# Performance work log

Measured on AMD Instinct MI355X. Metric: run time of the kernel, lower is better.

Reference implementation:

```python
import jax, jax.numpy as jnp
import numpy as np
from jax import lax

# ---- fixed configuration (matches init_kwargs / input_specs) ----
L, E, V, F, HU, HL, S = 32, 1024, 2048, 8, 128, 2, 7
D0, D1R, D1E = 512, 129, 640
D = S + 1                      # path dimension = num_slices + 1
SIGLEN = D + D * D + D * D * D # iisignature.siglength(8, 3) = 584
FINAL = F * 2 * SIGLEN         # 9344
EPS = 1e-5                     # BatchNorm eps


def _bn(x, g, b):
    # BatchNorm1d in training mode: biased batch statistics over axis 0
    mu = x.mean(0)
    var = x.var(0)
    return (x - mu) / jnp.sqrt(var + EPS) * g + b


def _mlp(x, Win, bin_, gin, betain, Wh, bh, gh, betah, Wout, bout, gout, betaout):
    # eigf: Linear+BN+ReLU blocks, 1 -> HU -> ... -> HU -> 1
    h = jax.nn.relu(_bn(x @ Win.T + bin_, gin, betain))
    for l in range(HL):
        h = jax.nn.relu(_bn(h @ Wh[l].T + bh[l], gh[l], betah[l]))
    o = jax.nn.relu(_bn(h @ Wout.T + bout, gout, betaout))
    return o[:, 0]


# ---- path signature, level 3, via Chen's identity (replaces iisignature.sig) ----
def _seg(dx):
    s1 = dx
    s2 = jnp.outer(s1, dx).reshape(-1) * 0.5
    s3 = jnp.outer(s2, dx).reshape(-1) / 3.0
    return (s1, s2, s3)


def _chen(Sg, T):
    s1, s2, s3 = Sg
    t1, t2, t3 = T
    r1 = s1 + t1
    r2 = s2 + t2 + jnp.outer(s1, t1).reshape(-1)
    r3 = s3 + t3 + jnp.outer(s1, t2).reshape(-1) + jnp.outer(s2, t1).reshape(-1)
    return (r1, r2, r3)


def _sig3(path):  # path [P, D] -> [SIGLEN]
    dX = path[1:] - path[:-1]

    def step(Sg, dx):
        return _chen(Sg, _seg(dx)), None

    Sg, _ = lax.scan(step, _seg(dX[0]), dX[1:])
    return jnp.concatenate(Sg)


def _diagram_sig(vals, W_proj, b_proj):
    # Conv1d(1, S, kernel=2, stride=2) == pairwise projection; then sort, prepend time axis
    pairs = vals.reshape(-1, 2)                      # [P, 2]
    P = pairs.shape[0]
    proj = jnp.einsum('pk,sk->sp', pairs, W_proj[:, 0, :]) + b_proj[:, None]  # [S, P]
    proj = jnp.sort(proj, axis=-1)
    t = jnp.arange(P, dtype=vals.dtype) / (P * (P + 1) / 2.0)
    path = jnp.concatenate([t[None, :], proj], axis=0).T  # [P, D]
    return _sig3(path)


def setup_inputs() -> dict:
    key = jax.random.key(0)
    ks = iter(jax.random.split(key, 16))
    nrm = lambda kk, shp, sc: jax.random.normal(kk, shp, jnp.float32) * sc
    inp = {
        "eigenvalues": jax.random.uniform(next(ks), (L, E), jnp.float32),
        "eigenvectors_sq": jax.random.uniform(next(ks), (L, E, V), jnp.float32) / E,
        "dgm0": jax.random.randint(next(ks), (L, F, D0), 0, V, jnp.int32),
        "dgm1rel": jax.random.randint(next(ks), (L, F, D1R), 0, V, jnp.int32),
        "dgm1ext": jax.random.randint(next(ks), (L, F, D1E), 0, V, jnp.int32),
        "mlp_Win": nrm(next(ks), (F, HU, 1), 1.0),
        "mlp_bin": jnp.zeros((F, HU), jnp.float32),
        "mlp_gin": jnp.ones((F, HU), jnp.float32),
        "mlp_betain": jnp.zeros((F, HU), jnp.float32),
        "mlp_Wh": nrm(next(ks), (F, HL, HU, HU), 1.0 / np.sqrt(HU)),
        "mlp_bh": jnp.zeros((F, HL, HU), jnp.float32),
        "mlp_gh": jnp.ones((F, HL, HU), jnp.float32),
        "mlp_betah": jnp.zeros((F, HL, HU), jnp.float32),
        "mlp_Wout": nrm(next(ks), (F, 1, HU), 1.0 / np.sqrt(HU)),
        "mlp_bout": jnp.zeros((F, 1), jnp.float32),
        "mlp_gout": jnp.ones((F, 1), jnp.float32),
        "mlp_betaout": jnp.zeros((F, 1), jnp.float32),
        "W_proj": nrm(next(ks), (S, 1, 2), 0.7),
        "b_proj": jnp.zeros((S,), jnp.float32),
        "W_fin": nrm(next(ks), (1, FINAL), 1.0 / np.sqrt(FINAL)),
        "b_fin": jnp.zeros((1,), jnp.float32),
        "g_fin": jnp.ones((1,), jnp.float32),
        "beta_fin": jnp.zeros((1,), jnp.float32),
    }
    return inp


def reference(eigenvalues, eigenvectors_sq, dgm0, dgm1rel, dgm1ext,
              mlp_Win, mlp_bin, mlp_gin, mlp_betain,
              mlp_Wh, mlp_bh, mlp_gh, mlp_betah,
              mlp_Wout, mlp_bout, mlp_gout, mlp_betaout,
              W_proj, b_proj, W_fin, b_fin, g_fin, beta_fin):
    flat = eigenvalues.reshape(-1, 1)  # [L*E, 1], sample-major like the torch flatten
    evs = jax.vmap(lambda *p: _mlp(flat, *p))(
        mlp_Win, mlp_bin, mlp_gin, mlp_betain,
        mlp_Wh, mlp_bh, mlp_gh, mlp_betah,
        mlp_Wout, mlp_bout, mlp_gout, mlp_betaout)  # [F, L*E]
    # per-sample filtration values: evs_transformed[:, slice_i] @ eigvecsq_i
    f = jnp.einsum('fle,lev->lfv', evs.reshape(F, L, E), eigenvectors_sq)  # [L, F, V]
    fv = f.reshape(L * F, V)
    d0 = jnp.take_along_axis(fv, dgm0.reshape(L * F, D0), axis=1)
    rel = jnp.take_along_axis(fv, dgm1rel.reshape(L * F, D1R), axis=1)
    # torch.arange(len-1, 0, -1): reversed, dropping element 0
    Dgm0 = jnp.concatenate([d0, rel[:, 1:][:, ::-1]], axis=1)  # [L*F, 640]
    Dgm1 = jnp.take_along_axis(fv, dgm1ext.reshape(L * F, D1E), axis=1)
    sig0 = jax.vmap(lambda v: _diagram_sig(v, W_proj, b_proj))(Dgm0)  # [L*F, SIGLEN]
    sig1 = jax.vmap(lambda v: _diagram_sig(v, W_proj, b_proj))(Dgm1)
    x = jnp.concatenate([sig0, sig1], axis=-1).reshape(L, FINAL)
    out = x @ W_fin.T + b_fin  # dropout p=0.0 -> identity
    return _bn(out, g_fin, beta_fin)  # [L, 1]
```

## Files before the change

### kernel.cpp

```cpp
#include <hip/hip_runtime.h>
#include <cfloat>
#include <math.h>

#define N_SAMP 32768
#define FF 8
#define HU 128
#define EE 1024
#define VV 2048
#define PP 320
#define SIGLEN 584
#define FINAL_W 9344

typedef unsigned short u16;
typedef unsigned int u32;
typedef short s16x8 __attribute__((ext_vector_type(8)));
typedef float f32x4 __attribute__((ext_vector_type(4)));

__device__ __forceinline__ u16 f2bf(float v) {
  u32 u = __float_as_uint(v);
  return (u16)((u + 0x7fffu + ((u >> 16) & 1u)) >> 16);
}
__device__ __forceinline__ float bf2f(u16 h) {
  return __uint_as_float(((u32)h) << 16);
}
__device__ __forceinline__ void split3(float v, u16& h, u16& m, u16& l) {
  h = f2bf(v);
  float r = v - bf2f(h);
  m = f2bf(r);
  float r2 = r - bf2f(m);
  l = f2bf(r2);
}

__device__ __forceinline__ double wave_red(double v) {
#pragma unroll
  for (int off = 32; off > 0; off >>= 1) v += __shfl_xor(v, off, 64);
  return v;
}

__global__ __launch_bounds__(256) void k_wsplit(const float* __restrict__ W,
                                                u16* __restrict__ Hh, u16* __restrict__ Hm,
                                                u16* __restrict__ Hl, int n) {
  int i = blockIdx.x * 256 + threadIdx.x;
  if (i >= n) return;
  u16 h, m, l;
  split3(W[i], h, m, l);
  Hh[i] = h; Hm[i] = m; Hl[i] = l;
}

__global__ __launch_bounds__(256) void k_xstats(const float* __restrict__ x,
                                                double* __restrict__ xst) {
  const int tid = threadIdx.x;
  double s1 = 0.0, s2 = 0.0;
  for (int i = tid; i < N_SAMP; i += 256) { double v = (double)x[i]; s1 += v; s2 += v * v; }
  __shared__ double r1[4], r2[4];
  double w1 = wave_red(s1), w2 = wave_red(s2);
  int wave = tid >> 6, lane = tid & 63;
  if (lane == 0) { r1[wave] = w1; r2[wave] = w2; }
  __syncthreads();
  if (tid == 0) {
    xst[0] = r1[0] + r1[1] + r1[2] + r1[3];
    xst[1] = r2[0] + r2[1] + r2[2] + r2[3];
  }
}

template<int MODE>
__global__ __launch_bounds__(256, 2)
void k_mgemm(const float* __restrict__ Ain,
             const double* __restrict__ xstats,
             const float* __restrict__ w_in,
             const float* __restrict__ g_in,
             const float* __restrict__ beta_in,
             const float* __restrict__ sc,
             const float* __restrict__ sh,
             const u16* __restrict__ Wh_,
             const u16* __restrict__ Wm_,
             const u16* __restrict__ Wl_,
             const float* __restrict__ bb, int bstride,
             float* __restrict__ Yt_out,
             double* __restrict__ stats) {
  __shared__ u16 SB[6][128 * 40];
  __shared__ float p0[HU], p1[HU], biasl[HU], xl[HU];
  u16* Ah = SB[0]; u16* Am = SB[1]; u16* Al = SB[2];
  u16* Bh = SB[3]; u16* Bm = SB[4]; u16* Bl = SB[5];

  const int tid = threadIdx.x;
  const int f = blockIdx.y;
  const int m0 = blockIdx.x * 128;
  const int lane = tid & 63, ln = tid & 15, quad = (tid >> 4) & 3, wave = tid >> 6;

  if (tid < HU) {
    biasl[tid] = bb[(size_t)f * bstride + tid];
    if (MODE == 0) {
      double mx = xstats[0] * (1.0 / 32768.0);
      double vx = xstats[1] * (1.0 / 32768.0) - mx * mx;
      if (vx < 0) vx = 0;
      float w = w_in[f * HU + tid];
      double inv = 1.0 / sqrt((double)w * (double)w * vx + 1e-5);
      float sj = (float)inv * g_in[f * HU + tid] * w;
      p0[tid] = sj;
      p1[tid] = beta_in[f * HU + tid] - (float)mx * sj;
      xl[tid] = Ain[m0 + tid];
    } else {
      p0[tid] = sc[f * HU + tid];
      p1[tid] = sh[f * HU + tid];
    }
  }

  f32x4 acc[2][8];
#pragma unroll
  for (int mt = 0; mt < 2; ++mt)
#pragma unroll
    for (int u = 0; u < 8; ++u) acc[mt][u] = (f32x4){0.f, 0.f, 0.f, 0.f};

  __syncthreads();

  for (int kk = 0; kk < 128; kk += 32) {
    if (MODE == 0) {
      const int m = tid >> 1, kh = (tid & 1) * 16;
      const float xv = xl[m];
      u32 ph[8], pm[8], pl[8];
#pragma unroll
      for (int jp = 0; jp < 8; ++jp) {
        u16 h0, m_0, l0, h1, m_1, l1;
        int k = kh + jp * 2;
        split3(fmaxf(fmaf(xv, p0[kk + k], p1[kk + k]), 0.f), h0, m_0, l0);
        split3(fmaxf(fmaf(xv, p0[kk + k + 1], p1[kk + k + 1]), 0.f), h1, m_1, l1);
        ph[jp] = (u32)h0 | ((u32)h1 << 16);
        pm[jp] = (u32)m_0 | ((u32)m_1 << 16);
        pl[jp] = (u32)l0 | ((u32)l1 << 16);
      }
      int off = m * 40 + kh;
      *(uint4*)&Ah[off] = make_uint4(ph[0], ph[1], ph[2], ph[3]);
      *(uint4*)&Ah[off + 8] = make_uint4(ph[4], ph[5], ph[6], ph[7]);
      *(uint4*)&Am[off] = make_uint4(pm[0], pm[1], pm[2], pm[3]);
      *(uint4*)&Am[off + 8] = make_uint4(pm[4], pm[5], pm[6], pm[7]);
      *(uint4*)&Al[off] = make_uint4(pl[0], pl[1], pl[2], pl[3]);
      *(uint4*)&Al[off + 8] = make_uint4(pl[4], pl[5], pl[6], pl[7]);
    } else {
#pragma unroll
      for (int r = 0; r < 4; ++r) {
        int flat = tid + r * 256;
        int m = flat & 127, kq = flat >> 7;
        const float* src = Ain + ((size_t)(f * HU + kk + kq * 4)) * N_SAMP + m0 + m;
        u32 ph[2], pm[2], pl[2];
#pragma unroll
        for (int ip = 0; ip < 2; ++ip) {
          int k = kq * 4 + ip * 2;
          float v0 = fmaxf(fmaf(src[(size_t)(ip * 2) * N_SAMP], p0[kk + k], p1[kk + k]), 0.f);
          float v1 = fmaxf(fmaf(src[(size_t)(ip * 2 + 1) * N_SAMP], p0[kk + k + 1], p1[kk + k + 1]), 0.f);
          u16 h0, m_0, l0, h1, m_1, l1;
          split3(v0, h0, m_0, l0);
          split3(v1, h1, m_1, l1);
          ph[ip] = (u32)h0 | ((u32)h1 << 16);
          pm[ip] = (u32)m_0 | ((u32)m_1 << 16);
          pl[ip] = (u32)l0 | ((u32)l1 << 16);
        }
        int off = m * 40 + kq * 4;
        *(uint2*)&Ah[off] = make_uint2(ph[0], ph[1]);
        *(uint2*)&Am[off] = make_uint2(pm[0], pm[1]);
        *(uint2*)&Al[off] = make_uint2(pl[0], pl[1]);
      }
    }
#pragma unroll
    for (int r = 0; r < 2; ++r) {
      int flat = tid + r * 256;
      int n = flat >> 2, c = flat & 3;
      size_t g = (size_t)f * (2 * HU * HU) + (size_t)n * HU + kk + c * 8;
      int off = n * 40 + c * 8;
      *(uint4*)&Bh[off] = *(const uint4*)&Wh_[g];
      *(uint4*)&Bm[off] = *(const uint4*)&Wm_[g];
      *(uint4*)&Bl[off] = *(const uint4*)&Wl_[g];
    }
    __syncthreads();
    s16x8 af0[3], af1[3];
    {
      int r0 = (wave * 32 + ln) * 40 + quad * 8;
      int r1 = (wave * 32 + 16 + ln) * 40 + quad * 8;
      af0[0] = *(const s16x8*)&Ah[r0]; af0[1] = *(const s16x8*)&Am[r0]; af0[2] = *(const s16x8*)&Al[r0];
      af1[0] = *(const s16x8*)&Ah[r1]; af1[1] = *(const s16x8*)&Am[r1]; af1[2] = *(const s16x8*)&Al[r1];
    }
#pragma unroll
    for (int u = 0; u < 8; ++u) {
      int bo = (u * 16 + ln) * 40 + quad * 8;
      s16x8 bh = *(const s16x8*)&Bh[bo];
      s16x8 bm = *(const s16x8*)&Bm[bo];
      s16x8 bl = *(const s16x8*)&Bl[bo];
      f32x4 a0 = acc[0][u], a1 = acc[1][u];
      a0 = __builtin_amdgcn_mfma_f32_16x16x32_bf16(af0[0], bh, a0, 0, 0, 0);
      a1 = __builtin_amdgcn_mfma_f32_16x16x32_bf16(af1[0], bh, a1, 0, 0, 0);
      a0 = __builtin_amdgcn_mfma_f32_16x16x32_bf16(af0[1], bh, a0, 0, 0, 0);
      a1 = __builtin_amdgcn_mfma_f32_16x16x32_bf16(af1[1], bh, a1, 0, 0, 0);
      a0 = __builtin_amdgcn_mfma_f32_16x16x32_bf16(af0[0], bm, a0, 0, 0, 0);
      a1 = __builtin_amdgcn_mfma_f32_16x16x32_bf16(af1[0], bm, a1, 0, 0, 0);
      a0 = __builtin_amdgcn_mfma_f32_16x16x32_bf16(af0[2], bh, a0, 0, 0, 0);
      a1 = __builtin_amdgcn_mfma_f32_16x16x32_bf16(af1[2], bh, a1, 0, 0, 0);
      a0 = __builtin_amdgcn_mfma_f32_16x16x32_bf16(af0[1], bm, a0, 0, 0, 0);
      a1 = __builtin_amdgcn_mfma_f32_16x16x32_bf16(af1[1], bm, a1, 0, 0, 0);
      a0 = __builtin_amdgcn_mfma_f32_16x16x32_bf16(af0[0], bl, a0, 0, 0, 0);
      a1 = __builtin_amdgcn_mfma_f32_16x16x32_bf16(af1[0], bl, a1, 0, 0, 0);
      acc[0][u] = a0; acc[1][u] = a1;
    }
    __syncthreads();
  }

  float cs1[8], cs2[8];
#pragma unroll
  for (int u = 0; u < 8; ++u) { cs1[u] = 0.f; cs2[u] = 0.f; }
#pragma unroll
  for (int u = 0; u < 8; ++u) {
    float b = biasl[u * 16 + ln];
#pragma unroll
    for (int mt = 0; mt < 2; ++mt) {
#pragma unroll
      for (int reg = 0; reg < 4; ++reg) {
        float v = acc[mt][u][reg] + b;
        acc[mt][u][reg] = v;
        cs1[u] += v;
        cs2[u] = fmaf(v, v, cs2[u]);
      }
      float4 st = make_float4(acc[mt][u][0], acc[mt][u][1], acc[mt][u][2], acc[mt][u][3]);
      *(float4*)&Yt_out[((size_t)(f * HU + u * 16 + ln)) * N_SAMP + m0 + wave * 32 + mt * 16 + quad * 4] = st;
    }
  }
  float* red1 = (float*)&SB[0][0];
  float* red2 = red1 + 2048;
  int wq = wave * 4 + quad;
#pragma unroll
  for (int u = 0; u < 8; ++u) {
    red1[wq * 128 + u * 16 + ln] = cs1[u];
    red2[wq * 128 + u * 16 + ln] = cs2[u];
  }
  __syncthreads();
  {
    int which = tid >> 7, n = tid & 127;
    const float* rp = which ? red2 : red1;
    float s = 0.f;
#pragma unroll
    for (int r = 0; r < 16; ++r) s += rp[r * 128 + n];
    atomicAdd(&stats[(f * HU + n) * 2 + which], (double)s);
  }
}

__global__ __launch_bounds__(256) void k_fin(const double* __restrict__ stats,
                                             const float* __restrict__ g,
                                             const float* __restrict__ beta,
                                             int per_f, int gstride, int count,
                                             float* __restrict__ sc, float* __restrict__ sh) {
  int idx = blockIdx.x * 256 + threadIdx.x;
  if (idx >= count) return;
  int f = idx / per_f, j = idx - f * per_f;
  double S1 = stats[idx * 2 + 0], S2 = stats[idx * 2 + 1];
  double mean = S1 * (1.0 / 32768.0);
  double var = S2 * (1.0 / 32768.0) - mean * mean;
  if (var < 0) var = 0;
  double inv = 1.0 / sqrt(var + 1e-5);
  float gg = g[f * gstride + j];
  float scv = (float)inv * gg;
  sc[idx] = scv;
  sh[idx] = beta[f * gstride + j] - (float)mean * scv;
}

__global__ __launch_bounds__(256, 4) void k_outlayer(const float* __restrict__ Yt,
                                                     const float* __restrict__ sc2,
                                                     const float* __restrict__ sh2,
                                                     const float* __restrict__ Wout,
                                                     const float* __restrict__ bout,
                                                     float* __restrict__ evs_pre,
                                                     double* __restrict__ stats3) {
  __shared__ float wj[HU], scl[HU], shl[HU];
  const int tid = threadIdx.x;
  const int f = blockIdx.y;
  const int i = blockIdx.x * 256 + tid;
  if (tid < HU) {
    wj[tid] = Wout[f * HU + tid];
    scl[tid] = sc2[f * HU + tid];
    shl[tid] = sh2[f * HU + tid];
  }
  __syncthreads();
  const float* base = Yt + (size_t)f * HU * N_SAMP + i;
  float acc = 0.f;
#pragma unroll
  for (int j = 0; j < HU; ++j) {
    float y = base[(size_t)j * N_SAMP];
    acc = fmaf(fmaxf(fmaf(y, scl[j], shl[j]), 0.f), wj[j], acc);
  }
  float yo = acc + bout[f];
  evs_pre[(size_t)f * N_SAMP + i] = yo;
  double v = (double)yo;
  double s1 = wave_red(v), s2 = wave_red(v * v);
  __shared__ double r1[4], r2[4];
  int wave = tid >> 6, lane = tid & 63;
  if (lane == 0) { r1[wave] = s1; r2[wave] = s2; }
  __syncthreads();
  if (tid == 0) atomicAdd(&stats3[f * 2 + 0], r1[0] + r1[1] + r1[2] + r1[3]);
  if (tid == 1) atomicAdd(&stats3[f * 2 + 1], r2[0] + r2[1] + r2[2] + r2[3]);
}

__global__ __launch_bounds__(256) void k_einsum(const float* __restrict__ evs_pre,
                                                const float* __restrict__ sc3,
                                                const float* __restrict__ sh3,
                                                const float* __restrict__ eig,
                                                float* __restrict__ fv) {
  __shared__ float ev[FF * EE];
  const int tid = threadIdx.x;
  const int l = blockIdx.y;
  const int v0 = blockIdx.x * 256;
#pragma unroll
  for (int r = 0; r < 32; ++r) {
    int q = tid + r * 256;
    int f = q >> 10, e = q & 1023;
    float y = evs_pre[(size_t)f * N_SAMP + l * EE + e];
    ev[q] = fmaxf(fmaf(y, sc3[f], sh3[f]), 0.f);
  }
  __syncthreads();
  const float* up = eig + (size_t)l * EE * VV + v0 + tid;
  float acc[8] = {0, 0, 0, 0, 0, 0, 0, 0};
  for (int e0 = 0; e0 < EE; e0 += 32) {
    float u[32];
#pragma unroll
    for (int t = 0; t < 32; ++t) u[t] = up[(size_t)(e0 + t) * VV];
#pragma unroll
    for (int t = 0; t < 32; ++t) {
#pragma unroll
      for (int f = 0; f < 8; ++f) acc[f] = fmaf(ev[f * EE + e0 + t], u[t], acc[f]);
    }
  }
#pragma unroll
  for (int f = 0; f < 8; ++f) fv[((size_t)(l * FF + f)) * VV + v0 + tid] = acc[f];
}

__global__ __launch_bounds__(256) void k_diagram(const float* __restrict__ fv,
                                                 const int* __restrict__ dgm0,
                                                 const int* __restrict__ dgm1rel,
                                                 const int* __restrict__ dgm1ext,
                                                 const float* __restrict__ Wp,
                                                 const float* __restrict__ bp,
                                                 float* __restrict__ xbuf) {
  __shared__ float vals[640];
  __shared__ float ps[7 * 512];
  __shared__ float dXl[320][8];
  const int tid = threadIdx.x;
  const int bid = blockIdx.x;
  const int row = bid >> 1;
  const int c = bid & 1;
  const float* fvr = fv + (size_t)row * VV;

  for (int k = tid; k < 640; k += 256) {
    int idx;
    if (c == 0) idx = (k < 512) ? dgm0[(size_t)row * 512 + k] : dgm1rel[(size_t)row * 129 + (640 - k)];
    else        idx = dgm1ext[(size_t)row * 640 + k];
    vals[k] = fvr[idx];
  }
  __syncthreads();
  for (int q = tid; q < 7 * 512; q += 256) {
    int s = q >> 9, p = q & 511;
    float pv = 3.402823466e+38f;
    if (p < PP) pv = fmaf(Wp[2 * s + 1], vals[2 * p + 1], fmaf(Wp[2 * s], vals[2 * p], bp[s]));
    ps[s * 512 + p] = pv;
  }
  for (int k = 2; k <= 512; k <<= 1) {
    for (int j = k >> 1; j > 0; j >>= 1) {
      __syncthreads();
      for (int q = tid; q < 1792; q += 256) {
        int s = q >> 8, ip = q & 255;
        int i = ((ip & ~(j - 1)) << 1) | (ip & (j - 1));
        int p2 = i | j;
        float a = ps[s * 512 + i], b = ps[s * 512 + p2];
        bool up = ((i & k) == 0);
        if ((a > b) == up) { ps[s * 512 + i] = b; ps[s * 512 + p2] = a; }
      }
    }
  }
  __syncthreads();
  for (int q = tid; q < 319 * 8; q += 256) {
    int p = q >> 3, d = q & 7;
    dXl[p][d] = (d == 0) ? (1.0f / 51360.0f)
                         : ps[(d - 1) * 512 + p + 1] - ps[(d - 1) * 512 + p];
  }
  __syncthreads();
  if (tid < 64) {
    const int a = tid >> 3, b = tid & 7;
    float s1a = 0.f, s2r = 0.f;
    float s3r[8] = {0, 0, 0, 0, 0, 0, 0, 0};
    for (int p = 0; p < 319; ++p) {
      float4 dlo = *(const float4*)&dXl[p][0];
      float4 dhi = *(const float4*)&dXl[p][4];
      float dxa = dXl[p][a];
      float dxb = dXl[p][b];
      float coefA = fmaf(dxa, (1.f / 3.f), s1a);
      float w = fmaf(0.5f * dxb, coefA, s2r);
      s2r = fmaf(dxb, fmaf(0.5f, dxa, s1a), s2r);
      s3r[0] = fmaf(w, dlo.x, s3r[0]);
      s3r[1] = fmaf(w, dlo.y, s3r[1]);
      s3r[2] = fmaf(w, dlo.z, s3r[2]);
      s3r[3] = fmaf(w, dlo.w, s3r[3]);
      s3r[4] = fmaf(w, dhi.x, s3r[4]);
      s3r[5] = fmaf(w, dhi.y, s3r[5]);
      s3r[6] = fmaf(w, dhi.z, s3r[6]);
      s3r[7] = fmaf(w, dhi.w, s3r[7]);
      s1a += dxa;
    }
    const int l = row >> 3, ff = row & 7;
    float* xr = xbuf + (size_t)l * FINAL_W + ff * (2 * SIGLEN) + c * SIGLEN;
    if ((tid & 7) == 0) xr[a] = s1a;
    xr[8 + tid] = s2r;
    float* s3p = xr + 72 + tid * 8;
    *(float4*)(s3p + 0) = make_float4(s3r[0], s3r[1], s3r[2], s3r[3]);
    *(float4*)(s3p + 4) = make_float4(s3r[4], s3r[5], s3r[6], s3r[7]);
  }
}

__global__ __launch_bounds__(256) void k_rowdot(const float* __restrict__ xbuf,
                                                const float* __restrict__ Wf,
                                                const float* __restrict__ bf,
                                                double* __restrict__ outpre) {
  const int tid = threadIdx.x, l = blockIdx.x;
  const float* xr = xbuf + (size_t)l * FINAL_W;
  double acc = 0.0;
  for (int k = tid; k < FINAL_W; k += 256) acc += (double)xr[k] * (double)Wf[k];
  acc = wave_red(acc);
  __shared__ double r[4];
  int wave = tid >> 6, lane = tid & 63;
  if (lane == 0) r[wave] = acc;
  __syncthreads();
  if (tid == 0) outpre[l] = r[0] + r[1] + r[2] + r[3] + (double)bf[0];
}

__global__ __launch_bounds__(64) void k_bnfin(const double* __restrict__ outpre,
                                              const float* __restrict__ g,
                                              const float* __restrict__ beta,
                                              float* __restrict__ dout) {
  int i = threadIdx.x;
  double v = (i < 32) ? outpre[i] : 0.0;
  double s1 = wave_red(v);
  double s2 = wave_red(v * v);
  double mean = s1 * (1.0 / 32.0);
  double var = s2 * (1.0 / 32.0) - mean * mean;
  if (var < 0) var = 0;
  double inv = 1.0 / sqrt(var + 1e-5);
  if (i < 32) dout[i] = (float)((v - mean) * inv * (double)g[0] + (double)beta[0]);
}

extern "C" void kernel_launch(void* const* d_in, const int* in_sizes, int n_in,
                              void* d_out, int out_size, void* d_ws, size_t ws_size,
                              hipStream_t stream) {
  const float* eig     = (const float*)d_in[0];
  const float* eigsq   = (const float*)d_in[1];
  const int*   dgm0    = (const int*)d_in[2];
  const int*   dgm1rel = (const int*)d_in[3];
  const int*   dgm1ext = (const int*)d_in[4];
  const float* Win     = (const float*)d_in[5];
  const float* gin     = (const float*)d_in[7];
  const float* betain  = (const float*)d_in[8];
  const float* Wh      = (const float*)d_in[9];
  const float* bh      = (const float*)d_in[10];
  const float* gh      = (const float*)d_in[11];
  const float* betah   = (const float*)d_in[12];
  const float* Wout    = (const float*)d_in[13];
  const float* bout    = (const float*)d_in[14];
  const float* gout    = (const float*)d_in[15];
  const float* betaout = (const float*)d_in[16];
  const float* Wp      = (const float*)d_in[17];
  const float* bp      = (const float*)d_in[18];
  const float* Wfin    = (const float*)d_in[19];
  const float* bfin    = (const float*)d_in[20];
  const float* gfin    = (const float*)d_in[21];
  const float* betafin = (const float*)d_in[22];

  char* ws = (char*)d_ws;
  float*  Yt      = (float*)(ws);
  float*  evs_pre = (float*)(ws + 134217728u);
  float*  fv      = (float*)(ws + 135266304u);
  float*  xbuf    = (float*)(ws + 137363456u);
  float*  sc1     = (float*)(ws + 138559488u);
  float*  sh1     = sc1 + 1024;
  float*  sc2     = sc1 + 2048;
  float*  sh2     = sc1 + 3072;
  float*  sc3     = sc1 + 4096;
  float*  sh3     = sc1 + 4160;
  double* stats1  = (double*)(ws + 138576384u);
  double* stats2  = stats1 + 2048;
  double* stats3  = stats1 + 4096;
  double* xstats  = stats1 + 4112;
  double* outpre  = stats1 + 4114;
  u16*    Whh     = (u16*)(ws + 138612736u);
  u16*    Whm     = (u16*)(ws + 139137024u);
  u16*    Whl     = (u16*)(ws + 139661312u);

  hipMemsetAsync(stats1, 0, 4114 * sizeof(double), stream);

  k_wsplit<<<1024, 256, 0, stream>>>(Wh, Whh, Whm, Whl, FF * 2 * HU * HU);
  k_xstats<<<1, 256, 0, stream>>>(eig, xstats);
  k_mgemm<0><<<dim3(256, FF), 256, 0, stream>>>(eig, xstats, Win, gin, betain,
                                                nullptr, nullptr,
                                                Whh, Whm, Whl,
                                                bh, 256, Yt, stats1);
  k_fin<<<4, 256, 0, stream>>>(stats1, gh, betah, 128, 256, 1024, sc1, sh1);
  k_mgemm<1><<<dim3(256, FF), 256, 0, stream>>>(Yt, nullptr, nullptr, nullptr, nullptr,
                                                sc1, sh1,
                                                Whh + HU * HU, Whm + HU * HU, Whl + HU * HU,
                                                bh + 128, 256, Yt, stats2);
  k_fin<<<4, 256, 0, stream>>>(stats2, gh + 128, betah + 128, 128, 256, 1024, sc2, sh2);
  k_outlayer<<<dim3(128, FF), 256, 0, stream>>>(Yt, sc2, sh2, Wout, bout, evs_pre, stats3);
  k_fin<<<1, 256, 0, stream>>>(stats3, gout, betaout, 1, 1, 8, sc3, sh3);
  k_einsum<<<dim3(8, 32), 256, 0, stream>>>(evs_pre, sc3, sh3, eigsq, fv);
  k_diagram<<<512, 256, 0, stream>>>(fv, dgm0, dgm1rel, dgm1ext, Wp, bp, xbuf);
  k_rowdot<<<32, 256, 0, stream>>>(xbuf, Wfin, bfin, outpre);
  k_bnfin<<<1, 64, 0, stream>>>(outpre, gfin, betafin, (float*)d_out);
}
```

Measured before the change: 745.8 us.

## Fold BN finalize kernels into consumers, merge prep launches, widen signature threads

Removes the memset, the separate weight-split and x-stats kernels, and the three k_fin launches. Their work moves into a single multi-role prep kernel, and each BN scale/shift is now computed inline in the consuming kernel's prologue. The x-stats reduction is split over 32 blocks instead of one serial block. In k_diagram all 256 threads now compute the level-3 signature loop, each handling 2 outputs instead of 8, where before only 64 threads did. This cuts launch overhead and serial tails, at the cost of some redundant per-block recomputation of the BN parameters.

```diff
diff --git a/kernel.cpp b/kernel.cpp
--- a/kernel.cpp
+++ b/kernel.cpp
@@ -37,41 +37,53 @@
   return v;
 }
 
-__global__ __launch_bounds__(256) void k_wsplit(const float* __restrict__ W,
-                                                u16* __restrict__ Hh, u16* __restrict__ Hm,
-                                                u16* __restrict__ Hl, int n) {
-  int i = blockIdx.x * 256 + threadIdx.x;
-  if (i >= n) return;
-  u16 h, m, l;
-  split3(W[i], h, m, l);
-  Hh[i] = h; Hm[i] = m; Hl[i] = l;
-}
-
-__global__ __launch_bounds__(256) void k_xstats(const float* __restrict__ x,
-                                                double* __restrict__ xst) {
-  const int tid = threadIdx.x;
-  double s1 = 0.0, s2 = 0.0;
-  for (int i = tid; i < N_SAMP; i += 256) { double v = (double)x[i]; s1 += v; s2 += v * v; }
+__global__ __launch_bounds__(256) void k_prep(const float* __restrict__ W,
+                                              u16* __restrict__ Hh, u16* __restrict__ Hm,
+                                              u16* __restrict__ Hl,
+                                              const float* __restrict__ x,
+                                              double* __restrict__ xp,
+                                              double* __restrict__ stats_zero) {
   __shared__ double r1[4], r2[4];
-  double w1 = wave_red(s1), w2 = wave_red(s2);
-  int wave = tid >> 6, lane = tid & 63;
-  if (lane == 0) { r1[wave] = w1; r2[wave] = w2; }
-  __syncthreads();
-  if (tid == 0) {
-    xst[0] = r1[0] + r1[1] + r1[2] + r1[3];
-    xst[1] = r2[0] + r2[1] + r2[2] + r2[3];
+  const int bid = blockIdx.x, tid = threadIdx.x;
+  if (bid < 1024) {
+    int i = bid * 256 + tid;
+    u16 h, m, l;
+    split3(W[i], h, m, l);
+    Hh[i] = h; Hm[i] = m; Hl[i] = l;
+  } else if (bid < 1056) {
+    int b = bid - 1024;
+    double s1 = 0.0, s2 = 0.0;
+    int base = b * 1024 + tid;
+#pragma unroll
+    for (int r = 0; r < 4; ++r) {
+      double v = (double)x[base + r * 256];
+      s1 += v; s2 += v * v;
+    }
+    s1 = wave_red(s1); s2 = wave_red(s2);
+    int wave = tid >> 6, lane = tid & 63;
+    if (lane == 0) { r1[wave] = s1; r2[wave] = s2; }
+    __syncthreads();
+    if (tid == 0) {
+      xp[b * 2 + 0] = r1[0] + r1[1] + r1[2] + r1[3];
+      xp[b * 2 + 1] = r2[0] + r2[1] + r2[2] + r2[3];
+    }
+  } else {
+    int q = (bid - 1056) * 256 + tid;
+    stats_zero[q] = 0.0;
+    if (bid == 1056 && tid < 16) stats_zero[4096 + tid] = 0.0;
   }
 }
 
 template<int MODE>
 __global__ __launch_bounds__(256, 2)
 void k_mgemm(const float* __restrict__ Ain,
-             const double* __restrict__ xstats,
+             const double* __restrict__ xp,
              const float* __restrict__ w_in,
              const float* __restrict__ g_in,
              const float* __restrict__ beta_in,
-             const float* __restrict__ sc,
-             const float* __restrict__ sh,
+             const double* __restrict__ stats_in,
+             const float* __restrict__ gM1,
+             const float* __restrict__ betaM1,
              const u16* __restrict__ Wh_,
              const u16* __restrict__ Wm_,
              const u16* __restrict__ Wl_,
@@ -91,8 +103,11 @@
   if (tid < HU) {
     biasl[tid] = bb[(size_t)f * bstride + tid];
     if (MODE == 0) {
-      double mx = xstats[0] * (1.0 / 32768.0);
-      double vx = xstats[1] * (1.0 / 32768.0) - mx * mx;
+      double S1 = 0.0, S2 = 0.0;
+#pragma unroll
+      for (int r = 0; r < 32; ++r) { S1 += xp[r * 2]; S2 += xp[r * 2 + 1]; }
+      double mx = S1 * (1.0 / 32768.0);
+      double vx = S2 * (1.0 / 32768.0) - mx * mx;
       if (vx < 0) vx = 0;
       float w = w_in[f * HU + tid];
       double inv = 1.0 / sqrt((double)w * (double)w * vx + 1e-5);
@@ -101,8 +116,16 @@
       p1[tid] = beta_in[f * HU + tid] - (float)mx * sj;
       xl[tid] = Ain[m0 + tid];
     } else {
-      p0[tid] = sc[f * HU + tid];
-      p1[tid] = sh[f * HU + tid];
+      int idx = f * HU + tid;
+      double S1 = stats_in[idx * 2 + 0], S2 = stats_in[idx * 2 + 1];
+      double mean = S1 * (1.0 / 32768.0);
+      double var = S2 * (1.0 / 32768.0) - mean * mean;
+      if (var < 0) var = 0;
+      double inv = 1.0 / sqrt(var + 1e-5);
+      float gg = gM1[f * 256 + tid];
+      float scv = (float)inv * gg;
+      p0[tid] = scv;
+      p1[tid] = betaM1[f * 256 + tid] - (float)mean * scv;
     }
   }
 
@@ -241,28 +264,10 @@
   }
 }
 
-__global__ __launch_bounds__(256) void k_fin(const double* __restrict__ stats,
-                                             const float* __restrict__ g,
-                                             const float* __restrict__ beta,
-                                             int per_f, int gstride, int count,
-                                             float* __restrict__ sc, float* __restrict__ sh) {
-  int idx = blockIdx.x * 256 + threadIdx.x;
-  if (idx >= count) return;
-  int f = idx / per_f, j = idx - f * per_f;
-  double S1 = stats[idx * 2 + 0], S2 = stats[idx * 2 + 1];
-  double mean = S1 * (1.0 / 32768.0);
-  double var = S2 * (1.0 / 32768.0) - mean * mean;
-  if (var < 0) var = 0;
-  double inv = 1.0 / sqrt(var + 1e-5);
-  float gg = g[f * gstride + j];
-  float scv = (float)inv * gg;
-  sc[idx] = scv;
-  sh[idx] = beta[f * gstride + j] - (float)mean * scv;
-}
-
 __global__ __launch_bounds__(256, 4) void k_outlayer(const float* __restrict__ Yt,
-                                                     const float* __restrict__ sc2,
-                                                     const float* __restrict__ sh2,
+                                                     const double* __restrict__ stats2,
+                                                     const float* __restrict__ gh,
+                                                     const float* __restrict__ betah,
                                                      const float* __restrict__ Wout,
                                                      const float* __restrict__ bout,
                                                      float* __restrict__ evs_pre,
@@ -273,8 +278,16 @@
   const int i = blockIdx.x * 256 + tid;
   if (tid < HU) {
     wj[tid] = Wout[f * HU + tid];
-    scl[tid] = sc2[f * HU + tid];
-    shl[tid] = sh2[f * HU + tid];
+    int idx = f * HU + tid;
+    double S1 = stats2[idx * 2 + 0], S2 = stats2[idx * 2 + 1];
+    double mean = S1 * (1.0 / 32768.0);
+    double var = S2 * (1.0 / 32768.0) - mean * mean;
+    if (var < 0) var = 0;
+    double inv = 1.0 / sqrt(var + 1e-5);
+    float gg = gh[128 + f * 256 + tid];
+    float scv = (float)inv * gg;
+    scl[tid] = scv;
+    shl[tid] = betah[128 + f * 256 + tid] - (float)mean * scv;
   }
   __syncthreads();
   const float* base = Yt + (size_t)f * HU * N_SAMP + i;
@@ -297,20 +310,34 @@
 }
 
 __global__ __launch_bounds__(256) void k_einsum(const float* __restrict__ evs_pre,
-                                                const float* __restrict__ sc3,
-                                                const float* __restrict__ sh3,
+                                                const double* __restrict__ stats3,
+                                                const float* __restrict__ gout,
+                                                const float* __restrict__ betaout,
                                                 const float* __restrict__ eig,
                                                 float* __restrict__ fv) {
   __shared__ float ev[FF * EE];
+  __shared__ float scl3[FF], shl3[FF];
   const int tid = threadIdx.x;
   const int l = blockIdx.y;
   const int v0 = blockIdx.x * 256;
+  if (tid < FF) {
+    double S1 = stats3[tid * 2 + 0], S2 = stats3[tid * 2 + 1];
+    double mean = S1 * (1.0 / 32768.0);
+    double var = S2 * (1.0 / 32768.0) - mean * mean;
+    if (var < 0) var = 0;
+    double inv = 1.0 / sqrt(var + 1e-5);
+    float gg = gout[tid];
+    float scv = (float)inv * gg;
+    scl3[tid] = scv;
+    shl3[tid] = betaout[tid] - (float)mean * scv;
+  }
+  __syncthreads();
 #pragma unroll
   for (int r = 0; r < 32; ++r) {
     int q = tid + r * 256;
     int f = q >> 10, e = q & 1023;
     float y = evs_pre[(size_t)f * N_SAMP + l * EE + e];
-    ev[q] = fmaxf(fmaf(y, sc3[f], sh3[f]), 0.f);
+    ev[q] = fmaxf(fmaf(y, scl3[f], shl3[f]), 0.f);
   }
   __syncthreads();
   const float* up = eig + (size_t)l * EE * VV + v0 + tid;
@@ -378,35 +405,27 @@
                          : ps[(d - 1) * 512 + p + 1] - ps[(d - 1) * 512 + p];
   }
   __syncthreads();
-  if (tid < 64) {
-    const int a = tid >> 3, b = tid & 7;
-    float s1a = 0.f, s2r = 0.f;
-    float s3r[8] = {0, 0, 0, 0, 0, 0, 0, 0};
+  {
+    const int a = tid >> 5, b = (tid >> 2) & 7, dp = tid & 3;
+    float s1a = 0.f, s2r = 0.f, s3r0 = 0.f, s3r1 = 0.f;
     for (int p = 0; p < 319; ++p) {
-      float4 dlo = *(const float4*)&dXl[p][0];
-      float4 dhi = *(const float4*)&dXl[p][4];
       float dxa = dXl[p][a];
       float dxb = dXl[p][b];
+      float2 dd = *(const float2*)&dXl[p][dp * 2];
       float coefA = fmaf(dxa, (1.f / 3.f), s1a);
       float w = fmaf(0.5f * dxb, coefA, s2r);
       s2r = fmaf(dxb, fmaf(0.5f, dxa, s1a), s2r);
-      s3r[0] = fmaf(w, dlo.x, s3r[0]);
-      s3r[1] = fmaf(w, dlo.y, s3r[1]);
-      s3r[2] = fmaf(w, dlo.z, s3r[2]);
-      s3r[3] = fmaf(w, dlo.w, s3r[3]);
-      s3r[4] = fmaf(w, dhi.x, s3r[4]);
-      s3r[5] = fmaf(w, dhi.y, s3r[5]);
-      s3r[6] = fmaf(w, dhi.z, s3r[6]);
-      s3r[7] = fmaf(w, dhi.w, s3r[7]);
+      s3r0 = fmaf(w, dd.x, s3r0);
+      s3r1 = fmaf(w, dd.y, s3r1);
       s1a += dxa;
     }
     const int l = row >> 3, ff = row & 7;
     float* xr = xbuf + (size_t)l * FINAL_W + ff * (2 * SIGLEN) + c * SIGLEN;
-    if ((tid & 7) == 0) xr[a] = s1a;
-    xr[8 + tid] = s2r;
-    float* s3p = xr + 72 + tid * 8;
-    *(float4*)(s3p + 0) = make_float4(s3r[0], s3r[1], s3r[2], s3r[3]);
-    *(float4*)(s3p + 4) = make_float4(s3r[4], s3r[5], s3r[6], s3r[7]);
+    if (b == 0 && dp == 0) xr[a] = s1a;
+    if (dp == 0) xr[8 + a * 8 + b] = s2r;
+    float* s3p = xr + 72 + (a * 8 + b) * 8 + dp * 2;
+    s3p[0] = s3r0;
+    s3p[1] = s3r1;
   }
 }
 
@@ -472,38 +491,27 @@
   float*  evs_pre = (float*)(ws + 134217728u);
   float*  fv      = (float*)(ws + 135266304u);
   float*  xbuf    = (float*)(ws + 137363456u);
-  float*  sc1     = (float*)(ws + 138559488u);
-  float*  sh1     = sc1 + 1024;
-  float*  sc2     = sc1 + 2048;
-  float*  sh2     = sc1 + 3072;
-  float*  sc3     = sc1 + 4096;
-  float*  sh3     = sc1 + 4160;
   double* stats1  = (double*)(ws + 138576384u);
   double* stats2  = stats1 + 2048;
   double* stats3  = stats1 + 4096;
-  double* xstats  = stats1 + 4112;
-  double* outpre  = stats1 + 4114;
+  double* xp      = stats1 + 4112;
+  double* outpre  = stats1 + 4176;
   u16*    Whh     = (u16*)(ws + 138612736u);
   u16*    Whm     = (u16*)(ws + 139137024u);
   u16*    Whl     = (u16*)(ws + 139661312u);
 
-  hipMemsetAsync(stats1, 0, 4114 * sizeof(double), stream);
-
-  k_wsplit<<<1024, 256, 0, stream>>>(Wh, Whh, Whm, Whl, FF * 2 * HU * HU);
-  k_xstats<<<1, 256, 0, stream>>>(eig, xstats);
-  k_mgemm<0><<<dim3(256, FF), 256, 0, stream>>>(eig, xstats, Win, gin, betain,
-                                                nullptr, nullptr,
+  k_prep<<<1072, 256, 0, stream>>>(Wh, Whh, Whm, Whl, eig, xp, stats1);
+  k_mgemm<0><<<dim3(256, FF), 256, 0, stream>>>(eig, xp, Win, gin, betain,
+                                                nullptr, nullptr, nullptr,
                                                 Whh, Whm, Whl,
                                                 bh, 256, Yt, stats1);
-  k_fin<<<4, 256, 0, stream>>>(stats1, gh, betah, 128, 256, 1024, sc1, sh1);
   k_mgemm<1><<<dim3(256, FF), 256, 0, stream>>>(Yt, nullptr, nullptr, nullptr, nullptr,
-                                                sc1, sh1,
+                                                stats1, gh, betah,
                                                 Whh + HU * HU, Whm + HU * HU, Whl + HU * HU,
                                                 bh + 128, 256, Yt, stats2);
-  k_fin<<<4, 256, 0, stream>>>(stats2, gh + 128, betah + 128, 128, 256, 1024, sc2, sh2);
-  k_outlayer<<<dim3(128, FF), 256, 0, stream>>>(Yt, sc2, sh2, Wout, bout, evs_pre, stats3);
-  k_fin<<<1, 256, 0, stream>>>(stats3, gout, betaout, 1, 1, 8, sc3, sh3);
-  k_einsum<<<dim3(8, 32), 256, 0, stream>>>(evs_pre, sc3, sh3, eigsq, fv);
+  k_outlayer<<<dim3(128, FF), 256, 0, stream>>>(Yt, stats2, gh, betah, Wout, bout,
+                                                evs_pre, stats3);
+  k_einsum<<<dim3(8, 32), 256, 0, stream>>>(evs_pre, stats3, gout, betaout, eigsq, fv);
   k_diagram<<<512, 256, 0, stream>>>(fv, dgm0, dgm1rel, dgm1ext, Wp, bp, xbuf);
   k_rowdot<<<32, 256, 0, stream>>>(xbuf, Wfin, bfin, outpre);
   k_bnfin<<<1, 64, 0, stream>>>(outpre, gfin, betafin, (float*)d_out);
```

Measured after the change: 688.7 us. -7.7%, faster.
